# Kernel tuning notes

Hardware: AMD Instinct MI355X
Metric: run time of the kernel (lower is better)

Reference implementation:

```python
import jax, jax.numpy as jnp
import numpy as np


def setup_inputs() -> dict:
    key = jax.random.key(0)
    ks = jax.random.split(key, 7)
    B, S, D = 256, 1024, 128  # batch of sets, set size, n_input
    H = 256
    x = jax.random.normal(ks[0], (B, S, D), dtype=jnp.float32)
    # torch nn.Linear weights: [out_features, in_features], in = 2*layer_in
    W0 = jax.random.normal(ks[1], (H, 2 * D), dtype=jnp.float32) * 0.05
    b0 = jnp.zeros((H,), dtype=jnp.float32)
    W1 = jax.random.normal(ks[2], (H, 2 * H), dtype=jnp.float32) * 0.05
    b1 = jnp.zeros((H,), dtype=jnp.float32)
    W2 = jax.random.normal(ks[3], (H, 2 * H), dtype=jnp.float32) * 0.05
    b2 = jnp.zeros((H,), dtype=jnp.float32)
    return {"x": x, "W0": W0, "b0": b0, "W1": W1, "b1": b1, "W2": W2, "b2": b2}


def reference(x, W0, b0, W1, b1, W2, b2):
    # x: [B, S, D] batch of sets. Original loops over batch; we vmap.
    def apply_set(y):
        # y: [S, d]
        for W, b in ((W0, b0), (W1, b1), (W2, b2)):
            mean = jnp.mean(y, axis=0, keepdims=True)            # [1, d]
            mean = jnp.broadcast_to(mean, y.shape)               # [S, d]
            z = jnp.concatenate([y, mean], axis=1)               # [S, 2d]
            y = jnp.tanh(z @ W.T + b)                            # [S, out]
        return jnp.mean(y, axis=0)                               # [out]
    return jax.vmap(apply_set)(x)                                # [B, out]
```

## Files before the change

### kernel.cpp

```cpp
#include <hip/hip_runtime.h>
#include <hip/hip_bf16.h>

#define B_ 256
#define S_ 1024
#define D_ 128
#define H_ 256

typedef short short8 __attribute__((ext_vector_type(8)));
typedef float f32x4 __attribute__((ext_vector_type(4)));

__device__ unsigned short g_Wb0[H_ * D_];
__device__ unsigned short g_Wb1[H_ * H_];
__device__ unsigned short g_Wb2[H_ * H_];
__device__ float g_mean0[B_ * D_];
__device__ float g_colsum1[B_ * H_];
__device__ float g_colsum2[B_ * H_];

__device__ __forceinline__ unsigned short f2bf(float x) {
    union { float f; unsigned u; } v; v.f = x;
    unsigned r = v.u + 0x7FFFu + ((v.u >> 16) & 1u);
    return (unsigned short)(r >> 16);
}
__device__ __forceinline__ float bf2f(unsigned short h) {
    union { float f; unsigned u; } v; v.u = ((unsigned)h) << 16;
    return v.f;
}
__device__ __forceinline__ float fast_tanh(float x) {
    float e = __builtin_amdgcn_exp2f(x * 2.885390081777927f);
    float r = __builtin_amdgcn_rcpf(1.0f + e);
    return 1.0f - 2.0f * r;
}

__global__ __launch_bounds__(256) void prep_kernel(
    const float* __restrict__ W0, const float* __restrict__ W1,
    const float* __restrict__ W2)
{
    int i = blockIdx.x * 256 + threadIdx.x;
    if (i < H_ * D_) { g_Wb0[i] = f2bf(W0[(i >> 7) * 256 + (i & 127)]); return; }
    i -= H_ * D_;
    if (i < H_ * H_) { g_Wb1[i] = f2bf(W1[(i >> 8) * 512 + (i & 255)]); return; }
    i -= H_ * H_;
    if (i < H_ * H_) { g_Wb2[i] = f2bf(W2[(i >> 8) * 512 + (i & 255)]); return; }
}

__global__ __launch_bounds__(1024) void means0_kernel(const float* __restrict__ x)
{
    const int set = blockIdx.x, t = threadIdx.x;
    const int cg = t & 31, rg = t >> 5;
    const float* xb = x + (size_t)set * S_ * D_;
    f32x4 s = (f32x4){0.f, 0.f, 0.f, 0.f};
    #pragma unroll 8
    for (int i = 0; i < 32; ++i)
        s += *(const f32x4*)(xb + (rg + i * 32) * D_ + cg * 4);
    __shared__ f32x4 red[32][32];
    red[rg][cg] = s;
    __syncthreads();
    if (t < 32) {
        f32x4 a = red[0][t];
        #pragma unroll
        for (int g = 1; g < 32; ++g) a += red[g][t];
        #pragma unroll
        for (int c = 0; c < 4; ++c) g_mean0[set * D_ + t * 4 + c] = a[c];
    }
}

template <int LAYER>
__global__ __launch_bounds__(512, 2) void layer_kernel(
    const float* __restrict__ x, const float* __restrict__ W,
    const float* __restrict__ bias, unsigned short* __restrict__ y,
    float* __restrict__ out)
{
    constexpr int K  = (LAYER == 0) ? D_ : H_;
    constexpr int KS = K / 32;
    constexpr int SLOTS = K / 8;
    const int set = blockIdx.x;
    const int t = threadIdx.x;
    const int lane = t & 63, wave = t >> 6;
    const int l15 = lane & 15, quad = lane >> 4;

    __shared__ unsigned short W_lds[256 * K];
    __shared__ float mean_lds[K];
    __shared__ float c_lds[H_];
    __shared__ float colsum_lds[H_];
    __shared__ float cpart[512];

    const unsigned short* Wb = (LAYER == 0) ? g_Wb0 : (LAYER == 1) ? g_Wb1 : g_Wb2;
    const float* msrc = (LAYER == 0) ? g_mean0 : (LAYER == 1) ? g_colsum1 : g_colsum2;

    if (t < K)   mean_lds[t] = msrc[set * K + t] * (1.f / S_);
    if (t < H_)  colsum_lds[t] = 0.f;
    __syncthreads();

    {
        const int n = t >> 1, h = t & 1;
        #pragma unroll
        for (int i = 0; i < SLOTS / 2; ++i) {
            const int slot = h * (SLOTS / 2) + i;
            *(uint4*)(&W_lds[n * K + ((slot ^ (n & 7)) * 8)]) =
                *(const uint4*)(&Wb[n * K + slot * 8]);
        }
    }
    {
        const int j = t >> 1, h = t & 1;
        const float* wl = W + j * 2 * K + h * (K / 2);
        const float* wr = wl + K;
        float acc = 0.f;
        #pragma unroll 4
        for (int k = 0; k < K / 2; k += 4) {
            f32x4 a = *(const f32x4*)(wl + k);
            f32x4 b = *(const f32x4*)(wr + k);
            f32x4 m = *(const f32x4*)(&mean_lds[h * (K / 2) + k]);
            #pragma unroll
            for (int c = 0; c < 4; ++c)
                acc += m[c] * (b[c] + (a[c] - bf2f(f2bf(a[c]))));
        }
        cpart[t] = acc;
    }
    __syncthreads();
    if (t < H_) c_lds[t] = bias[t] + cpart[2 * t] + cpart[2 * t + 1];
    __syncthreads();

    for (int half = 0; half < 2; ++half) {
        const int rowbase = half * 512 + wave * 64;

        short8 a[4][KS];
        if (LAYER == 0) {
            const float* xb = x + ((size_t)set * S_ + rowbase) * D_;
            #pragma unroll
            for (int mf = 0; mf < 4; ++mf)
                #pragma unroll
                for (int ks = 0; ks < KS; ++ks) {
                    const float* p = xb + (mf * 16 + l15) * D_ + ks * 32 + quad * 8;
                    f32x4 v0 = *(const f32x4*)(p);
                    f32x4 v1 = *(const f32x4*)(p + 4);
                    short8 sv;
                    #pragma unroll
                    for (int c = 0; c < 4; ++c) {
                        sv[c]     = (short)f2bf(v0[c]);
                        sv[4 + c] = (short)f2bf(v1[c]);
                    }
                    a[mf][ks] = sv;
                }
        } else {
            const unsigned short* yb = y + ((size_t)set * S_ + rowbase) * H_;
            #pragma unroll
            for (int mf = 0; mf < 4; ++mf)
                #pragma unroll
                for (int ks = 0; ks < KS; ++ks)
                    a[mf][ks] = *(const short8*)(yb + (mf * 16 + l15) * H_ + ks * 32 + quad * 8);
        }

        for (int nt = 0; nt < 8; ++nt) {
            f32x4 acc[4][2];
            #pragma unroll
            for (int i = 0; i < 4; ++i) {
                acc[i][0] = (f32x4){0.f, 0.f, 0.f, 0.f};
                acc[i][1] = (f32x4){0.f, 0.f, 0.f, 0.f};
            }
            const int r0 = (nt * 32 + l15) * K;
            const int r1 = (nt * 32 + 16 + l15) * K;
            #pragma unroll
            for (int ks = 0; ks < KS; ++ks) {
                const int so = (((ks * 4 + quad) ^ (l15 & 7)) * 8);
                short8 b0 = *(const short8*)(&W_lds[r0 + so]);
                short8 b1 = *(const short8*)(&W_lds[r1 + so]);
                #pragma unroll
                for (int mf = 0; mf < 4; ++mf)
                    acc[mf][0] = __builtin_amdgcn_mfma_f32_16x16x32_bf16(a[mf][ks], b0, acc[mf][0], 0, 0, 0);
                #pragma unroll
                for (int mf = 0; mf < 4; ++mf)
                    acc[mf][1] = __builtin_amdgcn_mfma_f32_16x16x32_bf16(a[mf][ks], b1, acc[mf][1], 0, 0, 0);
            }
            #pragma unroll
            for (int nf = 0; nf < 2; ++nf) {
                const int col = nt * 32 + nf * 16 + l15;
                const float cv = c_lds[col];
                float sn = 0.f;
                #pragma unroll
                for (int mf = 0; mf < 4; ++mf) {
                    #pragma unroll
                    for (int r = 0; r < 4; ++r) {
                        float th = fast_tanh(acc[mf][nf][r] + cv);
                        sn += th;
                        if (LAYER < 2)
                            y[((size_t)set * S_ + rowbase + mf * 16 + quad * 4 + r) * H_ + col] = f2bf(th);
                    }
                }
                sn += __shfl_xor(sn, 16);
                sn += __shfl_xor(sn, 32);
                if (quad == 0) atomicAdd(&colsum_lds[col], sn);
            }
        }
    }
    __syncthreads();
    if (t < H_) {
        if (LAYER == 2) out[set * H_ + t] = colsum_lds[t] * (1.f / S_);
        else if (LAYER == 1) g_colsum2[set * H_ + t] = colsum_lds[t];
        else g_colsum1[set * H_ + t] = colsum_lds[t];
    }
}

extern "C" void kernel_launch(void* const* d_in, const int* in_sizes, int n_in,
                              void* d_out, int out_size, void* d_ws, size_t ws_size,
                              hipStream_t stream) {
    (void)in_sizes; (void)n_in; (void)out_size; (void)ws_size;
    const float* x  = (const float*)d_in[0];
    const float* W0 = (const float*)d_in[1];
    const float* b0 = (const float*)d_in[2];
    const float* W1 = (const float*)d_in[3];
    const float* b1 = (const float*)d_in[4];
    const float* W2 = (const float*)d_in[5];
    const float* b2 = (const float*)d_in[6];
    float* out = (float*)d_out;
    unsigned short* ws = (unsigned short*)d_ws;

    prep_kernel<<<dim3(640), dim3(256), 0, stream>>>(W0, W1, W2);
    means0_kernel<<<dim3(256), dim3(1024), 0, stream>>>(x);
    layer_kernel<0><<<dim3(256), dim3(512), 0, stream>>>(x, W0, b0, ws, out);
    layer_kernel<1><<<dim3(256), dim3(512), 0, stream>>>(x, W1, b1, ws, out);
    layer_kernel<2><<<dim3(256), dim3(512), 0, stream>>>(x, W2, b2, ws, out);
}
```

Measured before the change: 443.0 us.

## Swap MFMA operands for vector stores, async LDS weight loads, precomputed fused weights

Several changes land together. The MFMA operands are swapped so each lane holds four consecutive output columns, which lets the tanh results be packed with v_cvt_pk_bf16 and written as 8-byte stores instead of scattered 2-byte stores. Column sums now go into a 16-way LDS table with atomics, replacing the shuffle reduction. Weights are pre-swizzled in prep, loaded with global_load_lds, and the mean-correction weight (b + a - bf16(a)) is precomputed once per layer rather than in every block. This adds extra global buffers and more LDS atomics.

```diff
diff --git a/kernel.cpp b/kernel.cpp
--- a/kernel.cpp
+++ b/kernel.cpp
@@ -1,5 +1,4 @@
 #include <hip/hip_runtime.h>
-#include <hip/hip_bf16.h>
 
 #define B_ 256
 #define S_ 1024
@@ -12,6 +11,9 @@
 __device__ unsigned short g_Wb0[H_ * D_];
 __device__ unsigned short g_Wb1[H_ * H_];
 __device__ unsigned short g_Wb2[H_ * H_];
+__device__ float g_Wc0[H_ * D_];
+__device__ float g_Wc1[H_ * H_];
+__device__ float g_Wc2[H_ * H_];
 __device__ float g_mean0[B_ * D_];
 __device__ float g_colsum1[B_ * H_];
 __device__ float g_colsum2[B_ * H_];
@@ -29,6 +31,16 @@
     float e = __builtin_amdgcn_exp2f(x * 2.885390081777927f);
     float r = __builtin_amdgcn_rcpf(1.0f + e);
     return 1.0f - 2.0f * r;
+}
+__device__ __forceinline__ unsigned cvt_pk_bf16(float lo, float hi) {
+    unsigned r;
+    asm("v_cvt_pk_bf16_f32 %0, %1, %2" : "=v"(r) : "v"(lo), "v"(hi));
+    return r;
+}
+__device__ __forceinline__ void gload_lds16(const unsigned short* g, unsigned short* l) {
+    __builtin_amdgcn_global_load_lds(
+        (const __attribute__((address_space(1))) void*)g,
+        (__attribute__((address_space(3))) void*)l, 16, 0, 0);
 }
 
 __global__ __launch_bounds__(256) void prep_kernel(
@@ -36,11 +48,24 @@
     const float* __restrict__ W2)
 {
     int i = blockIdx.x * 256 + threadIdx.x;
-    if (i < H_ * D_) { g_Wb0[i] = f2bf(W0[(i >> 7) * 256 + (i & 127)]); return; }
-    i -= H_ * D_;
-    if (i < H_ * H_) { g_Wb1[i] = f2bf(W1[(i >> 8) * 512 + (i & 255)]); return; }
-    i -= H_ * H_;
-    if (i < H_ * H_) { g_Wb2[i] = f2bf(W2[(i >> 8) * 512 + (i & 255)]); return; }
+    const float* W; unsigned short* wb; float* wc; int kbits;
+    if (i < H_ * D_) { W = W0; wb = g_Wb0; wc = g_Wc0; kbits = 7; }
+    else {
+        i -= H_ * D_;
+        if (i < H_ * H_) { W = W1; wb = g_Wb1; wc = g_Wc1; kbits = 8; }
+        else {
+            i -= H_ * H_;
+            if (i >= H_ * H_) return;
+            W = W2; wb = g_Wb2; wc = g_Wc2; kbits = 8;
+        }
+    }
+    const int K = 1 << kbits;
+    const int n = i >> kbits, k = i & (K - 1);
+    const float a = W[n * 2 * K + k];
+    const float b = W[n * 2 * K + K + k];
+    const unsigned short hb = f2bf(a);
+    wb[n * K + ((((k >> 3) ^ (n & 7)) << 3) | (k & 7))] = hb;
+    wc[n * K + k] = b + (a - bf2f(hb));
 }
 
 __global__ __launch_bounds__(1024) void means0_kernel(const float* __restrict__ x)
@@ -66,13 +91,11 @@
 
 template <int LAYER>
 __global__ __launch_bounds__(512, 2) void layer_kernel(
-    const float* __restrict__ x, const float* __restrict__ W,
-    const float* __restrict__ bias, unsigned short* __restrict__ y,
-    float* __restrict__ out)
+    const float* __restrict__ x, const float* __restrict__ bias,
+    unsigned short* __restrict__ y, float* __restrict__ out)
 {
     constexpr int K  = (LAYER == 0) ? D_ : H_;
     constexpr int KS = K / 32;
-    constexpr int SLOTS = K / 8;
     const int set = blockIdx.x;
     const int t = threadIdx.x;
     const int lane = t & 63, wave = t >> 6;
@@ -81,38 +104,35 @@
     __shared__ unsigned short W_lds[256 * K];
     __shared__ float mean_lds[K];
     __shared__ float c_lds[H_];
-    __shared__ float colsum_lds[H_];
     __shared__ float cpart[512];
+    __shared__ float colsum_t[16][257];
 
     const unsigned short* Wb = (LAYER == 0) ? g_Wb0 : (LAYER == 1) ? g_Wb1 : g_Wb2;
+    const float* Wc = (LAYER == 0) ? g_Wc0 : (LAYER == 1) ? g_Wc1 : g_Wc2;
     const float* msrc = (LAYER == 0) ? g_mean0 : (LAYER == 1) ? g_colsum1 : g_colsum2;
 
-    if (t < K)   mean_lds[t] = msrc[set * K + t] * (1.f / S_);
-    if (t < H_)  colsum_lds[t] = 0.f;
-    __syncthreads();
-
+    #pragma unroll
+    for (int i = t; i < 16 * 257; i += 512) (&colsum_t[0][0])[i] = 0.f;
+    if (t < K) mean_lds[t] = msrc[set * K + t] * (1.f / S_);
     {
-        const int n = t >> 1, h = t & 1;
-        #pragma unroll
-        for (int i = 0; i < SLOTS / 2; ++i) {
-            const int slot = h * (SLOTS / 2) + i;
-            *(uint4*)(&W_lds[n * K + ((slot ^ (n & 7)) * 8)]) =
-                *(const uint4*)(&Wb[n * K + slot * 8]);
-        }
-    }
+        constexpr int NCH = (256 * K * 2) / 1024;
+        #pragma unroll
+        for (int c = wave; c < NCH; c += 8)
+            gload_lds16(Wb + c * 512 + lane * 8, &W_lds[c * 512]);
+    }
+    __syncthreads();
+
     {
         const int j = t >> 1, h = t & 1;
-        const float* wl = W + j * 2 * K + h * (K / 2);
-        const float* wr = wl + K;
+        const float* wr = Wc + j * K + h * (K / 2);
+        const float* mr = &mean_lds[h * (K / 2)];
         float acc = 0.f;
         #pragma unroll 4
         for (int k = 0; k < K / 2; k += 4) {
-            f32x4 a = *(const f32x4*)(wl + k);
-            f32x4 b = *(const f32x4*)(wr + k);
-            f32x4 m = *(const f32x4*)(&mean_lds[h * (K / 2) + k]);
-            #pragma unroll
-            for (int c = 0; c < 4; ++c)
-                acc += m[c] * (b[c] + (a[c] - bf2f(f2bf(a[c]))));
+            f32x4 w = *(const f32x4*)(wr + k);
+            f32x4 m = *(const f32x4*)(mr + k);
+            #pragma unroll
+            for (int c = 0; c < 4; ++c) acc += m[c] * w[c];
         }
         cpart[t] = acc;
     }
@@ -133,13 +153,12 @@
                     const float* p = xb + (mf * 16 + l15) * D_ + ks * 32 + quad * 8;
                     f32x4 v0 = *(const f32x4*)(p);
                     f32x4 v1 = *(const f32x4*)(p + 4);
-                    short8 sv;
-                    #pragma unroll
-                    for (int c = 0; c < 4; ++c) {
-                        sv[c]     = (short)f2bf(v0[c]);
-                        sv[4 + c] = (short)f2bf(v1[c]);
-                    }
-                    a[mf][ks] = sv;
+                    union { short8 s; unsigned u[4]; } sv;
+                    sv.u[0] = cvt_pk_bf16(v0[0], v0[1]);
+                    sv.u[1] = cvt_pk_bf16(v0[2], v0[3]);
+                    sv.u[2] = cvt_pk_bf16(v1[0], v1[1]);
+                    sv.u[3] = cvt_pk_bf16(v1[2], v1[3]);
+                    a[mf][ks] = sv.s;
                 }
         } else {
             const unsigned short* yb = y + ((size_t)set * S_ + rowbase) * H_;
@@ -149,6 +168,8 @@
                 for (int ks = 0; ks < KS; ++ks)
                     a[mf][ks] = *(const short8*)(yb + (mf * 16 + l15) * H_ + ks * 32 + quad * 8);
         }
+
+        unsigned short* ybase = y + ((size_t)set * S_ + rowbase) * H_;
 
         for (int nt = 0; nt < 8; ++nt) {
             f32x4 acc[4][2];
@@ -158,45 +179,53 @@
                 acc[i][1] = (f32x4){0.f, 0.f, 0.f, 0.f};
             }
             const int r0 = (nt * 32 + l15) * K;
-            const int r1 = (nt * 32 + 16 + l15) * K;
+            const int r1 = r0 + 16 * K;
             #pragma unroll
             for (int ks = 0; ks < KS; ++ks) {
                 const int so = (((ks * 4 + quad) ^ (l15 & 7)) * 8);
-                short8 b0 = *(const short8*)(&W_lds[r0 + so]);
-                short8 b1 = *(const short8*)(&W_lds[r1 + so]);
+                short8 w0 = *(const short8*)(&W_lds[r0 + so]);
+                short8 w1 = *(const short8*)(&W_lds[r1 + so]);
                 #pragma unroll
                 for (int mf = 0; mf < 4; ++mf)
-                    acc[mf][0] = __builtin_amdgcn_mfma_f32_16x16x32_bf16(a[mf][ks], b0, acc[mf][0], 0, 0, 0);
+                    acc[mf][0] = __builtin_amdgcn_mfma_f32_16x16x32_bf16(w0, a[mf][ks], acc[mf][0], 0, 0, 0);
                 #pragma unroll
                 for (int mf = 0; mf < 4; ++mf)
-                    acc[mf][1] = __builtin_amdgcn_mfma_f32_16x16x32_bf16(a[mf][ks], b1, acc[mf][1], 0, 0, 0);
+                    acc[mf][1] = __builtin_amdgcn_mfma_f32_16x16x32_bf16(w1, a[mf][ks], acc[mf][1], 0, 0, 0);
             }
             #pragma unroll
             for (int nf = 0; nf < 2; ++nf) {
-                const int col = nt * 32 + nf * 16 + l15;
-                const float cv = c_lds[col];
-                float sn = 0.f;
+                const int colbase = nt * 32 + nf * 16 + quad * 4;
+                const f32x4 cv = *(const f32x4*)(&c_lds[colbase]);
+                f32x4 cs = (f32x4){0.f, 0.f, 0.f, 0.f};
                 #pragma unroll
                 for (int mf = 0; mf < 4; ++mf) {
+                    f32x4 th;
                     #pragma unroll
-                    for (int r = 0; r < 4; ++r) {
-                        float th = fast_tanh(acc[mf][nf][r] + cv);
-                        sn += th;
-                        if (LAYER < 2)
-                            y[((size_t)set * S_ + rowbase + mf * 16 + quad * 4 + r) * H_ + col] = f2bf(th);
+                    for (int r = 0; r < 4; ++r)
+                        th[r] = fast_tanh(acc[mf][nf][r] + cv[r]);
+                    cs += th;
+                    if (LAYER < 2) {
+                        uint2 pv;
+                        pv.x = cvt_pk_bf16(th[0], th[1]);
+                        pv.y = cvt_pk_bf16(th[2], th[3]);
+                        *(uint2*)(&ybase[(mf * 16 + l15) * H_ + colbase]) = pv;
                     }
                 }
-                sn += __shfl_xor(sn, 16);
-                sn += __shfl_xor(sn, 32);
-                if (quad == 0) atomicAdd(&colsum_lds[col], sn);
+                atomicAdd(&colsum_t[l15][colbase + 0], cs[0]);
+                atomicAdd(&colsum_t[l15][colbase + 1], cs[1]);
+                atomicAdd(&colsum_t[l15][colbase + 2], cs[2]);
+                atomicAdd(&colsum_t[l15][colbase + 3], cs[3]);
             }
         }
     }
     __syncthreads();
     if (t < H_) {
-        if (LAYER == 2) out[set * H_ + t] = colsum_lds[t] * (1.f / S_);
-        else if (LAYER == 1) g_colsum2[set * H_ + t] = colsum_lds[t];
-        else g_colsum1[set * H_ + t] = colsum_lds[t];
+        float v = 0.f;
+        #pragma unroll
+        for (int g = 0; g < 16; ++g) v += colsum_t[g][t];
+        if (LAYER == 2)      out[set * H_ + t] = v * (1.f / S_);
+        else if (LAYER == 1) g_colsum2[set * H_ + t] = v;
+        else                 g_colsum1[set * H_ + t] = v;
     }
 }
 
@@ -216,7 +245,7 @@
 
     prep_kernel<<<dim3(640), dim3(256), 0, stream>>>(W0, W1, W2);
     means0_kernel<<<dim3(256), dim3(1024), 0, stream>>>(x);
-    layer_kernel<0><<<dim3(256), dim3(512), 0, stream>>>(x, W0, b0, ws, out);
-    layer_kernel<1><<<dim3(256), dim3(512), 0, stream>>>(x, W1, b1, ws, out);
-    layer_kernel<2><<<dim3(256), dim3(512), 0, stream>>>(x, W2, b2, ws, out);
-}
+    layer_kernel<0><<<dim3(256), dim3(512), 0, stream>>>(x, b0, ws, out);
+    layer_kernel<1><<<dim3(256), dim3(512), 0, stream>>>(x, b1, ws, out);
+    layer_kernel<2><<<dim3(256), dim3(512), 0, stream>>>(x, b2, ws, out);
+}
```

Result: slower. 565.9 us (+27.7%).
